# Optimization experiments

Measured on AMD Instinct MI355X. Metric: run time of the kernel, lower is better.

Reference implementation:

```python
import jax, jax.numpy as jnp
import numpy as np

NEG_SLOPE = 0.2   # PyG GATConv default negative_slope
BN_EPS = 1e-5


def gat_conv(x, W, att_src, att_dst, bias, src, dst, num_nodes, concat):
    """PyG-style GATConv (eval mode, no dropout). att_*: [H, C]."""
    H, C = att_src.shape
    h = (x @ W).reshape(-1, H, C)                       # [N, H, C]
    a_src = jnp.sum(h * att_src[None], axis=-1)         # [N, H]
    a_dst = jnp.sum(h * att_dst[None], axis=-1)         # [N, H]
    e = jax.nn.leaky_relu(a_src[src] + a_dst[dst], NEG_SLOPE)  # [E, H]
    # segment softmax over incoming edges of each dst node
    m = jax.ops.segment_max(e, dst, num_segments=num_nodes)
    m = jnp.where(jnp.isfinite(m), m, 0.0)
    p = jnp.exp(e - m[dst])
    s = jax.ops.segment_sum(p, dst, num_segments=num_nodes)
    alpha = p / (s[dst] + 1e-16)                        # [E, H]
    msg = h[src] * alpha[:, :, None]                    # [E, H, C]
    out = jax.ops.segment_sum(msg, dst, num_segments=num_nodes)  # [N, H, C]
    out = out.reshape(num_nodes, H * C) if concat else out.mean(axis=1)
    return out + bias


def bn_eval(x, gamma, beta, mean, var):
    return (x - mean) * jax.lax.rsqrt(var + BN_EPS) * gamma + beta


def setup_inputs() -> dict:
    N, E = 50000, 800000
    IN, HID, HEADS, OUT = 22, 64, 4, 32
    key = jax.random.key(0)
    ks = jax.random.split(key, 12)
    d = {}
    d["x"] = jax.random.normal(ks[0], (N, IN), dtype=jnp.float32)
    d["edge_index"] = jax.random.randint(ks[1], (2, E), 0, N, dtype=jnp.int64)
    d["W1"] = jax.random.normal(ks[2], (IN, HEADS * HID), dtype=jnp.float32) * 0.2
    d["att_src1"] = jax.random.normal(ks[3], (HEADS, HID), dtype=jnp.float32) * 0.1
    d["att_dst1"] = jax.random.normal(ks[4], (HEADS, HID), dtype=jnp.float32) * 0.1
    d["b1"] = jnp.zeros((HEADS * HID,), dtype=jnp.float32)
    # GAT layer 2: 256 -> 32, 1 head, no concat (mean)
    d["W2"] = jax.random.normal(ks[5], (HEADS * HID, OUT), dtype=jnp.float32) * 0.06
    d["att_src2"] = jax.random.normal(ks[6], (1, OUT), dtype=jnp.float32) * 0.1
    d["att_dst2"] = jax.random.normal(ks[7], (1, OUT), dtype=jnp.float32) * 0.1
    d["b2"] = jnp.zeros((OUT,), dtype=jnp.float32)
    # BatchNorm params (eval mode)
    d["gamma1"] = jnp.ones((HEADS * HID,), dtype=jnp.float32)
    d["beta1"] = jnp.zeros((HEADS * HID,), dtype=jnp.float32)
    d["mean1"] = jax.random.normal(ks[8], (HEADS * HID,), dtype=jnp.float32) * 0.05
    d["var1"] = jnp.ones((HEADS * HID,), dtype=jnp.float32)
    d["gamma2"] = jnp.ones((OUT,), dtype=jnp.float32)
    d["beta2"] = jnp.zeros((OUT,), dtype=jnp.float32)
    d["mean2"] = jax.random.normal(ks[9], (OUT,), dtype=jnp.float32) * 0.05
    d["var2"] = jnp.ones((OUT,), dtype=jnp.float32)
    return d


def reference(x, edge_index, W1, att_src1, att_dst1, b1, W2, att_src2, att_dst2, b2,
              gamma1, beta1, mean1, var1, gamma2, beta2, mean2, var2):
    N = x.shape[0]
    # PyG GATConv adds self-loops by default
    loops = jnp.arange(N, dtype=edge_index.dtype)
    src = jnp.concatenate([edge_index[0], loops])
    dst = jnp.concatenate([edge_index[1], loops])
    h = gat_conv(x, W1, att_src1, att_dst1, b1, src, dst, N, concat=True)
    h = jax.nn.elu(bn_eval(h, gamma1, beta1, mean1, var1))
    # dropout: identity in eval mode
    h = gat_conv(h, W2, att_src2, att_dst2, b2, src, dst, N, concat=False)
    h = jax.nn.elu(bn_eval(h, gamma2, beta2, mean2, var2))
    return h
```

## Files before the change

### kernel.cpp

```cpp
#include <hip/hip_runtime.h>
#include <hip/hip_fp16.h>
#include <math.h>

#define NN   50000
#define EE   800000
#define ETOT 850000
#define INF_FEATS 22
#define D1   256
#define NH   4
#define D2   32
#define BN_EPS 1e-5f
#define NEG_SLOPE 0.2f
#define SCAN_B 49
#define AB_ROWS 8
#define AB_BLOCKS (NN / AB_ROWS)
#define CNT_BLOCKS ((ETOT + 255) / 256)

typedef _Float16 f16x8 __attribute__((ext_vector_type(8)));
typedef float f32x4 __attribute__((ext_vector_type(4)));

__device__ __forceinline__ float2 h2f(unsigned u) {
    __half2 h = *reinterpret_cast<__half2*>(&u);
    return __half22float2(h);
}

__global__ __launch_bounds__(128) void prep(const float* __restrict__ W1,
                                            const float* __restrict__ atts,
                                            const float* __restrict__ attd,
                                            float* __restrict__ WAs,
                                            float* __restrict__ WAd) {
    const int t = threadIdx.x;
    if (t >= INF_FEATS * NH) return;
    const int k = t >> 2, h = t & 3;
    float s = 0.f, d = 0.f;
    for (int c = 0; c < 64; ++c) {
        const float w = W1[k * D1 + h * 64 + c];
        s = fmaf(w, atts[h * 64 + c], s);
        d = fmaf(w, attd[h * 64 + c], d);
    }
    WAs[k * NH + h] = s;
    WAd[k * NH + h] = d;
}

__global__ __launch_bounds__(256) void sAB_count(
    const float* __restrict__ x, const float* __restrict__ W1,
    const float* __restrict__ WAs, const float* __restrict__ WAd,
    const int* __restrict__ ei, __half* __restrict__ h1h,
    float* __restrict__ as1, float* __restrict__ ad1,
    int* __restrict__ cnt, int* __restrict__ rank) {
    if (blockIdx.x >= AB_BLOCKS) {
        const int e = (blockIdx.x - AB_BLOCKS) * 256 + threadIdx.x;
        if (e < ETOT) {
            int dst = (e < EE) ? ei[EE + e] : (e - EE);
            rank[e] = atomicAdd(&cnt[dst], 1);
        }
        return;
    }
    __shared__ float xs[AB_ROWS][INF_FEATS];
    const int t = threadIdx.x;
    const int n0 = blockIdx.x * AB_ROWS;
    for (int i = t; i < AB_ROWS * INF_FEATS; i += 256)
        xs[i / INF_FEATS][i % INF_FEATS] = x[n0 * INF_FEATS + i];
    __syncthreads();
    float acc[AB_ROWS];
#pragma unroll
    for (int r = 0; r < AB_ROWS; ++r) acc[r] = 0.f;
#pragma unroll
    for (int k = 0; k < INF_FEATS; ++k) {
        const float wv = W1[k * D1 + t];
#pragma unroll
        for (int r = 0; r < AB_ROWS; ++r) acc[r] = fmaf(xs[r][k], wv, acc[r]);
    }
#pragma unroll
    for (int r = 0; r < AB_ROWS; ++r)
        h1h[(size_t)(n0 + r) * D1 + t] = __float2half(acc[r]);
    if (t < AB_ROWS * NH * 2) {
        const int r = t >> 3, idx = t & 7, h = idx >> 1;
        const float* WA = (idx & 1) ? WAd : WAs;
        float a = 0.f;
#pragma unroll
        for (int k = 0; k < INF_FEATS; ++k)
            a = fmaf(xs[r][k], WA[k * NH + h], a);
        ((idx & 1) ? ad1 : as1)[(n0 + r) * NH + h] = a;
    }
}

__global__ __launch_bounds__(1024) void scan_a(const int* __restrict__ cnt,
                                               int* __restrict__ offs,
                                               int* __restrict__ bsum) {
    __shared__ int sh[1024];
    const int t = threadIdx.x, i = blockIdx.x * 1024 + t;
    const int v = (i < NN) ? cnt[i] : 0;
    sh[t] = v;
    __syncthreads();
    for (int off = 1; off < 1024; off <<= 1) {
        int u = (t >= off) ? sh[t - off] : 0;
        __syncthreads();
        sh[t] += u;
        __syncthreads();
    }
    if (i < NN) offs[i] = sh[t] - v;
    if (t == 1023) bsum[blockIdx.x] = sh[1023];
}

__global__ __launch_bounds__(1024) void scan_c(int* __restrict__ offs,
                                               const int* __restrict__ bsum) {
    __shared__ int sbase;
    if (threadIdx.x == 0) {
        int r = 0;
        for (int b = 0; b < blockIdx.x; ++b) r += bsum[b];
        sbase = r;
    }
    __syncthreads();
    const int i = blockIdx.x * 1024 + threadIdx.x;
    if (i < NN) offs[i] += sbase;
    if (i == 0) offs[NN] = ETOT;
}

__global__ void c_scatter2(const int* __restrict__ ei,
                           const int* __restrict__ offs,
                           const int* __restrict__ rank,
                           int* __restrict__ ssrc) {
    int e = blockIdx.x * blockDim.x + threadIdx.x;
    if (e >= ETOT) return;
    int src, dst;
    if (e < EE) { src = ei[e]; dst = ei[EE + e]; }
    else        { src = dst = e - EE; }
    ssrc[offs[dst] + rank[e]] = src;
}

__global__ __launch_bounds__(256) void g1k(
    const uint2* __restrict__ h1q, const float* __restrict__ as1,
    const float* __restrict__ ad1, const int* __restrict__ offs,
    const int* __restrict__ ssrc, const float* __restrict__ b1,
    const float* __restrict__ g1, const float* __restrict__ be1,
    const float* __restrict__ mu1, const float* __restrict__ va1,
    uint2* __restrict__ hposth) {
    const int wv = threadIdx.x >> 6, lane = threadIdx.x & 63;
    const int n = blockIdx.x * 4 + wv;
    const int off = offs[n];
    const int deg = offs[n + 1] - off;
    const int h = lane >> 4;
    const float adst = ad1[n * NH + h];
    float a0 = 0.f, a1 = 0.f, a2 = 0.f, a3 = 0.f, ssum = 0.f;
    for (int p = 0; p < deg; p += 8) {
        int sj[8];
        float al[8];
#pragma unroll
        for (int u = 0; u < 8; ++u)
            sj[u] = (p + u < deg) ? ssrc[off + p + u] : ssrc[off];
#pragma unroll
        for (int u = 0; u < 8; ++u) {
            float a = as1[sj[u] * NH + h] + adst;
            a = (a >= 0.f) ? a : NEG_SLOPE * a;
            al[u] = (p + u < deg) ? __expf(a) : 0.f;
        }
        uint2 hv[8];
#pragma unroll
        for (int u = 0; u < 8; ++u)
            hv[u] = h1q[(size_t)sj[u] * 64 + lane];
#pragma unroll
        for (int u = 0; u < 8; ++u) {
            ssum += al[u];
            const float2 f0 = h2f(hv[u].x), f1 = h2f(hv[u].y);
            a0 = fmaf(al[u], f0.x, a0);
            a1 = fmaf(al[u], f0.y, a1);
            a2 = fmaf(al[u], f1.x, a2);
            a3 = fmaf(al[u], f1.y, a3);
        }
    }
    const float inv = 1.f / (ssum + 1e-16f);
    const float4 bb = ((const float4*)b1)[lane];
    const float4 mm = ((const float4*)mu1)[lane];
    const float4 vv = ((const float4*)va1)[lane];
    const float4 gg = ((const float4*)g1)[lane];
    const float4 ee = ((const float4*)be1)[lane];
    float4 o;
    o.x = (a0 * inv + bb.x - mm.x) * rsqrtf(vv.x + BN_EPS) * gg.x + ee.x;
    o.y = (a1 * inv + bb.y - mm.y) * rsqrtf(vv.y + BN_EPS) * gg.y + ee.y;
    o.z = (a2 * inv + bb.z - mm.z) * rsqrtf(vv.z + BN_EPS) * gg.z + ee.z;
    o.w = (a3 * inv + bb.w - mm.w) * rsqrtf(vv.w + BN_EPS) * gg.w + ee.w;
    o.x = (o.x > 0.f) ? o.x : expm1f(o.x);
    o.y = (o.y > 0.f) ? o.y : expm1f(o.y);
    o.z = (o.z > 0.f) ? o.z : expm1f(o.z);
    o.w = (o.w > 0.f) ? o.w : expm1f(o.w);
    __half2 p01 = __floats2half2_rn(o.x, o.y);
    __half2 p23 = __floats2half2_rn(o.z, o.w);
    uint2 st;
    st.x = *reinterpret_cast<unsigned*>(&p01);
    st.y = *reinterpret_cast<unsigned*>(&p23);
    hposth[(size_t)n * 64 + lane] = st;
}

__global__ __launch_bounds__(256) void sFGm(
    const uint4* __restrict__ hq,
    const float* __restrict__ W2,
    const float* __restrict__ atts, const float* __restrict__ attd,
    __half* __restrict__ h2h, float* __restrict__ as2, float* __restrict__ ad2) {
    const int w = threadIdx.x >> 6, l = threadIdx.x & 63;
    const int row0 = blockIdx.x * 64 + w * 16;
    const int lmod = l & 15, ldiv = l >> 4;
    f16x8 b0[8], b1[8];
#pragma unroll
    for (int ks = 0; ks < 8; ++ks) {
#pragma unroll
        for (int j = 0; j < 8; ++j) {
            const int k = ks * 32 + ldiv * 8 + j;
            b0[ks][j] = (_Float16)W2[k * D2 + lmod];
            b1[ks][j] = (_Float16)W2[k * D2 + lmod + 16];
        }
    }
    f32x4 acc0 = {0.f, 0.f, 0.f, 0.f}, acc1 = {0.f, 0.f, 0.f, 0.f};
    const int arow = min(row0 + lmod, NN - 1);
    const uint4* ap = hq + (size_t)arow * 32 + ldiv;
#pragma unroll
    for (int ks = 0; ks < 8; ++ks) {
        uint4 av = ap[ks * 4];
        f16x8 a = *reinterpret_cast<f16x8*>(&av);
        acc0 = __builtin_amdgcn_mfma_f32_16x16x32_f16(a, b0[ks], acc0, 0, 0, 0);
        acc1 = __builtin_amdgcn_mfma_f32_16x16x32_f16(a, b1[ks], acc1, 0, 0, 0);
    }
    const float a2s0 = atts[lmod], a2s1 = atts[lmod + 16];
    const float a2d0 = attd[lmod], a2d1 = attd[lmod + 16];
#pragma unroll
    for (int i = 0; i < 4; ++i) {
        const int r = row0 + ldiv * 4 + i;
        const bool ok = r < NN;
        if (ok) {
            h2h[(size_t)r * D2 + lmod]      = __float2half(acc0[i]);
            h2h[(size_t)r * D2 + lmod + 16] = __float2half(acc1[i]);
        }
        float s = acc0[i] * a2s0 + acc1[i] * a2s1;
        float d = acc0[i] * a2d0 + acc1[i] * a2d1;
#pragma unroll
        for (int m = 8; m > 0; m >>= 1) {
            s += __shfl_xor(s, m);
            d += __shfl_xor(d, m);
        }
        if (ok && lmod == 0) { as2[r] = s; ad2[r] = d; }
    }
}

__global__ __launch_bounds__(256) void g2k(
    const unsigned short* __restrict__ h2u, const float* __restrict__ as2,
    const float* __restrict__ ad2, const int* __restrict__ offs,
    const int* __restrict__ ssrc, const float* __restrict__ b2,
    const float* __restrict__ g2, const float* __restrict__ be2,
    const float* __restrict__ mu2, const float* __restrict__ va2,
    float* __restrict__ out) {
    const int t = threadIdx.x;
    const int n = blockIdx.x * 8 + (t >> 5), c = t & 31;
    const int off = offs[n];
    const int deg = offs[n + 1] - off;
    const float adst = ad2[n];
    float ssum = 0.f, acc = 0.f;
    for (int p = 0; p < deg; p += 8) {
        int sj[8];
        float al[8];
#pragma unroll
        for (int u = 0; u < 8; ++u)
            sj[u] = (p + u < deg) ? ssrc[off + p + u] : ssrc[off];
#pragma unroll
        for (int u = 0; u < 8; ++u) {
            float a = as2[sj[u]] + adst;
            a = (a >= 0.f) ? a : NEG_SLOPE * a;
            al[u] = (p + u < deg) ? __expf(a) : 0.f;
        }
        unsigned short hv[8];
#pragma unroll
        for (int u = 0; u < 8; ++u)
            hv[u] = h2u[sj[u] * D2 + c];
#pragma unroll
        for (int u = 0; u < 8; ++u) {
            ssum += al[u];
            acc = fmaf(al[u], __half2float(*reinterpret_cast<__half*>(&hv[u])), acc);
        }
    }
    float v = acc / (ssum + 1e-16f) + b2[c];
    v = (v - mu2[c]) * rsqrtf(va2[c] + BN_EPS) * g2[c] + be2[c];
    v = (v > 0.f) ? v : expm1f(v);
    out[n * D2 + c] = v;
}

extern "C" void kernel_launch(void* const* d_in, const int* in_sizes, int n_in,
                              void* d_out, int out_size, void* d_ws, size_t ws_size,
                              hipStream_t stream) {
    (void)in_sizes; (void)n_in; (void)out_size; (void)ws_size;
    const float* x    = (const float*)d_in[0];
    const int*   ei   = (const int*)  d_in[1];
    const float* W1   = (const float*)d_in[2];
    const float* as1i = (const float*)d_in[3];
    const float* ad1i = (const float*)d_in[4];
    const float* b1   = (const float*)d_in[5];
    const float* W2   = (const float*)d_in[6];
    const float* as2i = (const float*)d_in[7];
    const float* ad2i = (const float*)d_in[8];
    const float* b2   = (const float*)d_in[9];
    const float* g1   = (const float*)d_in[10];
    const float* be1  = (const float*)d_in[11];
    const float* mu1  = (const float*)d_in[12];
    const float* va1  = (const float*)d_in[13];
    const float* g2   = (const float*)d_in[14];
    const float* be2  = (const float*)d_in[15];
    const float* mu2  = (const float*)d_in[16];
    const float* va2  = (const float*)d_in[17];
    float* out = (float*)d_out;

    float* ws = (float*)d_ws;
    __half* hposth = (__half*)ws;
    float* as1  = ws + (size_t)NN * (D1 / 2);
    float* ad1  = as1 + (size_t)NN * NH;
    float* as2  = ad1 + (size_t)NN * NH;
    float* ad2  = as2 + NN;
    __half* h1h = (__half*)(ad2 + NN);
    __half* h2h = h1h + (size_t)NN * D1;
    int* cnt   = (int*)(h2h + (size_t)NN * D2);
    int* offs  = cnt + NN;
    int* rank  = offs + NN + 1;
    int* ssrc  = rank + ETOT;
    int* bsum  = ssrc + ETOT;
    float* WAs = (float*)(bsum + SCAN_B);
    float* WAd = WAs + INF_FEATS * NH;

    hipMemsetAsync(cnt, 0, NN * sizeof(int), stream);

    prep<<<1, 128, 0, stream>>>(W1, as1i, ad1i, WAs, WAd);
    sAB_count<<<AB_BLOCKS + CNT_BLOCKS, 256, 0, stream>>>(
        x, W1, WAs, WAd, ei, h1h, as1, ad1, cnt, rank);
    scan_a<<<SCAN_B, 1024, 0, stream>>>(cnt, offs, bsum);
    scan_c<<<SCAN_B, 1024, 0, stream>>>(offs, bsum);
    c_scatter2<<<(ETOT + 255) / 256, 256, 0, stream>>>(ei, offs, rank, ssrc);
    g1k<<<NN / 4, 256, 0, stream>>>((const uint2*)h1h, as1, ad1, offs, ssrc,
                                    b1, g1, be1, mu1, va1, (uint2*)hposth);
    sFGm<<<(NN + 63) / 64, 256, 0, stream>>>((const uint4*)hposth, W2,
                                             as2i, ad2i, h2h, as2, ad2);
    g2k<<<NN / 8, 256, 0, stream>>>((const unsigned short*)h2h, as2, ad2, offs,
                                    ssrc, b2, g2, be2, mu2, va2, out);
}
```

Before: 292.5 us.

## Fuse memset into prep, merge scan passes with decoupled lookback, reorder gathers

Replaces the hipMemset and the single-block prep kernel with one prep2 kernel that zeroes the count array and the scan flags while computing the W·att projections. The two-pass scan (scan_a plus scan_c) becomes a single scan_f kernel in which each block publishes its total through a flag and spins on the flags of its predecessors. In both gather kernels the feature loads are issued before the attention-score loads and exp, and launch bounds ask for 4 blocks per SM. The goal is fewer kernel launches and more memory-level parallelism. The spin-wait scan depends on all 49 blocks being co-resident, which holds on this GPU.

```diff
diff --git a/kernel.cpp b/kernel.cpp
--- a/kernel.cpp
+++ b/kernel.cpp
@@ -24,22 +24,30 @@
     return __half22float2(h);
 }
 
-__global__ __launch_bounds__(128) void prep(const float* __restrict__ W1,
-                                            const float* __restrict__ atts,
-                                            const float* __restrict__ attd,
-                                            float* __restrict__ WAs,
-                                            float* __restrict__ WAd) {
-    const int t = threadIdx.x;
-    if (t >= INF_FEATS * NH) return;
-    const int k = t >> 2, h = t & 3;
-    float s = 0.f, d = 0.f;
-    for (int c = 0; c < 64; ++c) {
-        const float w = W1[k * D1 + h * 64 + c];
-        s = fmaf(w, atts[h * 64 + c], s);
-        d = fmaf(w, attd[h * 64 + c], d);
-    }
-    WAs[k * NH + h] = s;
-    WAd[k * NH + h] = d;
+__global__ __launch_bounds__(1024) void prep2(const float* __restrict__ W1,
+                                              const float* __restrict__ atts,
+                                              const float* __restrict__ attd,
+                                              float* __restrict__ WAs,
+                                              float* __restrict__ WAd,
+                                              int* __restrict__ cnt,
+                                              int* __restrict__ flags) {
+    const int i = blockIdx.x * 1024 + threadIdx.x;
+    if (i < NN) cnt[i] = 0;
+    if (blockIdx.x == 0) {
+        const int t = threadIdx.x;
+        if (t < SCAN_B) flags[t] = 0;
+        if (t >= 128 && t < 128 + INF_FEATS * NH) {
+            const int k = (t - 128) >> 2, h = (t - 128) & 3;
+            float s = 0.f, d = 0.f;
+            for (int c = 0; c < 64; ++c) {
+                const float w = W1[k * D1 + h * 64 + c];
+                s = fmaf(w, atts[h * 64 + c], s);
+                d = fmaf(w, attd[h * 64 + c], d);
+            }
+            WAs[k * NH + h] = s;
+            WAd[k * NH + h] = d;
+        }
+    }
 }
 
 __global__ __launch_bounds__(256) void sAB_count(
@@ -85,11 +93,12 @@
     }
 }
 
-__global__ __launch_bounds__(1024) void scan_a(const int* __restrict__ cnt,
+__global__ __launch_bounds__(1024) void scan_f(const int* __restrict__ cnt,
                                                int* __restrict__ offs,
-                                               int* __restrict__ bsum) {
+                                               int* __restrict__ flags) {
     __shared__ int sh[1024];
-    const int t = threadIdx.x, i = blockIdx.x * 1024 + t;
+    __shared__ int sbase;
+    const int b = blockIdx.x, t = threadIdx.x, i = b * 1024 + t;
     const int v = (i < NN) ? cnt[i] : 0;
     sh[t] = v;
     __syncthreads();
@@ -99,21 +108,18 @@
         sh[t] += u;
         __syncthreads();
     }
-    if (i < NN) offs[i] = sh[t] - v;
-    if (t == 1023) bsum[blockIdx.x] = sh[1023];
-}
-
-__global__ __launch_bounds__(1024) void scan_c(int* __restrict__ offs,
-                                               const int* __restrict__ bsum) {
-    __shared__ int sbase;
-    if (threadIdx.x == 0) {
-        int r = 0;
-        for (int b = 0; b < blockIdx.x; ++b) r += bsum[b];
-        sbase = r;
+    if (t == 1023) atomicExch(&flags[b], sh[1023] + 1);
+    if (t == 0) {
+        int base = 0;
+        for (int j = 0; j < b; ++j) {
+            int f;
+            while ((f = atomicAdd(&flags[j], 0)) == 0) { }
+            base += f - 1;
+        }
+        sbase = base;
     }
     __syncthreads();
-    const int i = blockIdx.x * 1024 + threadIdx.x;
-    if (i < NN) offs[i] += sbase;
+    if (i < NN) offs[i] = sbase + sh[t] - v;
     if (i == 0) offs[NN] = ETOT;
 }
 
@@ -129,7 +135,7 @@
     ssrc[offs[dst] + rank[e]] = src;
 }
 
-__global__ __launch_bounds__(256) void g1k(
+__global__ __launch_bounds__(256, 4) void g1k(
     const uint2* __restrict__ h1q, const float* __restrict__ as1,
     const float* __restrict__ ad1, const int* __restrict__ offs,
     const int* __restrict__ ssrc, const float* __restrict__ b1,
@@ -145,20 +151,20 @@
     float a0 = 0.f, a1 = 0.f, a2 = 0.f, a3 = 0.f, ssum = 0.f;
     for (int p = 0; p < deg; p += 8) {
         int sj[8];
-        float al[8];
 #pragma unroll
         for (int u = 0; u < 8; ++u)
             sj[u] = (p + u < deg) ? ssrc[off + p + u] : ssrc[off];
+        uint2 hv[8];
+#pragma unroll
+        for (int u = 0; u < 8; ++u)
+            hv[u] = h1q[(size_t)sj[u] * 64 + lane];
+        float al[8];
 #pragma unroll
         for (int u = 0; u < 8; ++u) {
             float a = as1[sj[u] * NH + h] + adst;
             a = (a >= 0.f) ? a : NEG_SLOPE * a;
             al[u] = (p + u < deg) ? __expf(a) : 0.f;
         }
-        uint2 hv[8];
-#pragma unroll
-        for (int u = 0; u < 8; ++u)
-            hv[u] = h1q[(size_t)sj[u] * 64 + lane];
 #pragma unroll
         for (int u = 0; u < 8; ++u) {
             ssum += al[u];
@@ -241,7 +247,7 @@
     }
 }
 
-__global__ __launch_bounds__(256) void g2k(
+__global__ __launch_bounds__(256, 4) void g2k(
     const unsigned short* __restrict__ h2u, const float* __restrict__ as2,
     const float* __restrict__ ad2, const int* __restrict__ offs,
     const int* __restrict__ ssrc, const float* __restrict__ b2,
@@ -256,20 +262,20 @@
     float ssum = 0.f, acc = 0.f;
     for (int p = 0; p < deg; p += 8) {
         int sj[8];
-        float al[8];
 #pragma unroll
         for (int u = 0; u < 8; ++u)
             sj[u] = (p + u < deg) ? ssrc[off + p + u] : ssrc[off];
+        unsigned short hv[8];
+#pragma unroll
+        for (int u = 0; u < 8; ++u)
+            hv[u] = h2u[sj[u] * D2 + c];
+        float al[8];
 #pragma unroll
         for (int u = 0; u < 8; ++u) {
             float a = as2[sj[u]] + adst;
             a = (a >= 0.f) ? a : NEG_SLOPE * a;
             al[u] = (p + u < deg) ? __expf(a) : 0.f;
         }
-        unsigned short hv[8];
-#pragma unroll
-        for (int u = 0; u < 8; ++u)
-            hv[u] = h2u[sj[u] * D2 + c];
 #pragma unroll
         for (int u = 0; u < 8; ++u) {
             ssum += al[u];
@@ -318,17 +324,14 @@
     int* offs  = cnt + NN;
     int* rank  = offs + NN + 1;
     int* ssrc  = rank + ETOT;
-    int* bsum  = ssrc + ETOT;
-    float* WAs = (float*)(bsum + SCAN_B);
+    int* flags = ssrc + ETOT;
+    float* WAs = (float*)(flags + SCAN_B);
     float* WAd = WAs + INF_FEATS * NH;
 
-    hipMemsetAsync(cnt, 0, NN * sizeof(int), stream);
-
-    prep<<<1, 128, 0, stream>>>(W1, as1i, ad1i, WAs, WAd);
+    prep2<<<SCAN_B, 1024, 0, stream>>>(W1, as1i, ad1i, WAs, WAd, cnt, flags);
     sAB_count<<<AB_BLOCKS + CNT_BLOCKS, 256, 0, stream>>>(
         x, W1, WAs, WAd, ei, h1h, as1, ad1, cnt, rank);
-    scan_a<<<SCAN_B, 1024, 0, stream>>>(cnt, offs, bsum);
-    scan_c<<<SCAN_B, 1024, 0, stream>>>(offs, bsum);
+    scan_f<<<SCAN_B, 1024, 0, stream>>>(cnt, offs, flags);
     c_scatter2<<<(ETOT + 255) / 256, 256, 0, stream>>>(ei, offs, rank, ssrc);
     g1k<<<NN / 4, 256, 0, stream>>>((const uint2*)h1h, as1, ad1, offs, ssrc,
                                     b1, g1, be1, mu1, va1, (uint2*)hposth);
```

New measurement: 307.5 us. +5.1%, slower.
